# Performance work log

Hardware: AMD Instinct MI355X
Metric: run time of the kernel (lower is better)

The kernel has to match this reference:

```python
import jax, jax.numpy as jnp
import numpy as np

B, D, H, W, C_IN, F = 32, 8, 8, 8, 512, 96
KS = (3, 3, 3)


def setup_inputs() -> dict:
    key = jax.random.key(0)
    ks = jax.random.split(key, 12)
    sc_w = 0.05  # keras 'random_uniform' is small; scale keeps activations sane
    inp = {
        "inputs": jax.random.normal(ks[0], (B, C_IN), jnp.float32),
        "h_t": jax.random.normal(ks[1], (B, D, H, W, F), jnp.float32),
        "s_t": jax.random.normal(ks[2], (B, D, H, W, F), jnp.float32),
        "Wf": jax.random.uniform(ks[3], (D, H, W, C_IN, F), jnp.float32, -sc_w, sc_w),
        "Wi": jax.random.uniform(ks[4], (D, H, W, C_IN, F), jnp.float32, -sc_w, sc_w),
        "Ws": jax.random.uniform(ks[5], (D, H, W, C_IN, F), jnp.float32, -sc_w, sc_w),
        "Uf": jax.random.normal(ks[6], KS + (F, F), jnp.float32) * 0.05,
        "Ui": jax.random.normal(ks[7], KS + (F, F), jnp.float32) * 0.05,
        "Us": jax.random.normal(ks[8], KS + (F, F), jnp.float32) * 0.05,
        "bf": jnp.zeros((F,), jnp.float32),
        "bi": jnp.zeros((F,), jnp.float32),
        "bs": jnp.zeros((F,), jnp.float32),
    }
    return inp


def _conv3d_same(h, U):
    # channels_last 3D conv, stride 1, SAME padding (matches K.conv3d)
    return jax.lax.conv_general_dilated(
        h, U, window_strides=(1, 1, 1), padding="SAME",
        dimension_numbers=("NDHWC", "DHWIO", "NDHWC"))


def _hard_sigmoid(x):
    # keras hard_sigmoid: clip(0.2*x + 0.5, 0, 1)
    return jnp.clip(0.2 * x + 0.5, 0.0, 1.0)


def reference(inputs, h_t, s_t, Wf, Uf, Wi, Ui, Ws, Us, bf, bi, bs):
    # K.dot(inputs, W): contract input channel c against W's second-to-last axis
    def gate(Wg, Ug, bg):
        return jnp.einsum("bc,dhwcf->bdhwf", inputs, Wg) + _conv3d_same(h_t, Ug) + bg

    f = _hard_sigmoid(gate(Wf, Uf, bf))
    i = _hard_sigmoid(gate(Wi, Ui, bi))
    s = f * s_t + i * jnp.tanh(gate(Ws, Us, bs))
    h = jnp.tanh(s)
    return (h, s)
```

## Files before the change

### kernel.cpp

```cpp
#include <hip/hip_runtime.h>

typedef __attribute__((ext_vector_type(8))) short short8;
typedef __attribute__((ext_vector_type(4))) float f32x4;

constexpr int B_ = 32, C_ = 512, F_ = 96, P_ = 512;
constexpr int NTH = 768;
constexpr int GRID = 256;
constexpr size_t OUT_HALF = (size_t)B_ * P_ * F_;

constexpr size_t WS_U  = 0;
constexpr size_t WS_U_SZ = 27ull * 3 * 96 * 52 * 4;
constexpr size_t WS_H  = WS_U + WS_U_SZ;
constexpr size_t WS_H_SZ = 32ull * 512 * 96 * 2;
constexpr size_t WS_X  = WS_H + WS_H_SZ;
constexpr size_t WS_X_SZ = 32ull * 512 * 2;
constexpr size_t WS_END = WS_X + WS_X_SZ;

constexpr int SH_OFF = 0;
constexpr int SH_BUF = 64 * 208;
constexpr int SU_OFF = SH_OFF + 2 * SH_BUF;
constexpr int SU_BUF = 3 * 96 * 208;
constexpr int LDS_TOTAL = SU_OFF + 2 * SU_BUF;
constexpr int SX_OFF = 0;
constexpr int SW_OFF = 33280;
constexpr int SW_BUF = 6 * 96 * 80;
constexpr int PRE_OFF = 0;

__device__ __forceinline__ unsigned short f2bf(float v) {
    unsigned int u = __float_as_uint(v);
    unsigned int r = (u + 0x7FFFu + ((u >> 16) & 1u)) >> 16;
    return (unsigned short)r;
}
__device__ __forceinline__ unsigned pack2bf(float a, float b) {
    return (unsigned)f2bf(a) | ((unsigned)f2bf(b) << 16);
}
__device__ __forceinline__ float bf2f(unsigned short v) {
    return __uint_as_float(((unsigned int)v) << 16);
}

__global__ __launch_bounds__(256) void prep_u(const float* __restrict__ Uf,
                                              const float* __restrict__ Ui,
                                              const float* __restrict__ Us,
                                              unsigned char* __restrict__ wsb) {
    __shared__ float s32[96 * 97];
    const int t = blockIdx.x / 3, g = blockIdx.x % 3;
    const float* U = (g == 0 ? Uf : (g == 1 ? Ui : Us)) + (size_t)t * 9216;
    const int tid = threadIdx.x;
    #pragma unroll
    for (int j = 0; j < 36; ++j) {
        int idx = j * 256 + tid;
        int ci = idx / 96, f = idx % 96;
        s32[ci * 97 + f] = U[idx];
    }
    __syncthreads();
    unsigned* dst = (unsigned*)(wsb + WS_U) + (size_t)(t * 3 + g) * 4992;
    #pragma unroll
    for (int j = 0; j < 20; ++j) {
        int o = j * 256 + tid;
        if (o < 4992) {
            int f = o / 52, qq = o % 52;
            unsigned pk = 0u;
            if (qq < 48) pk = pack2bf(s32[(2 * qq) * 97 + f], s32[(2 * qq + 1) * 97 + f]);
            dst[o] = pk;
        }
    }
}

__global__ __launch_bounds__(256) void prep_hx(const float* __restrict__ h_t,
                                               const float* __restrict__ x,
                                               unsigned char* __restrict__ wsb) {
    unsigned* wh = (unsigned*)(wsb + WS_H);
    unsigned* wx = (unsigned*)(wsb + WS_X);
    const int tid = threadIdx.x;
    #pragma unroll
    for (int j = 0; j < 4; ++j) {
        size_t u = (size_t)blockIdx.x * 1024 + j * 256 + tid;
        if (u < 786432) {
            float2 v = *(const float2*)(h_t + 2 * u);
            wh[u] = pack2bf(v.x, v.y);
        } else if (u < 794624) {
            size_t v_ = u - 786432;
            float2 v = *(const float2*)(x + 2 * v_);
            wx[v_] = pack2bf(v.x, v.y);
        }
    }
}

__global__ __launch_bounds__(NTH, 3) void lstm3d_main(
    const float* __restrict__ Wf, const float* __restrict__ Wi, const float* __restrict__ Ws,
    const float* __restrict__ s_t,
    const float* __restrict__ bfp, const float* __restrict__ bip, const float* __restrict__ bsp,
    const unsigned char* __restrict__ wsb, float* __restrict__ out)
{
    extern __shared__ char sm[];
    const int tid  = threadIdx.x;
    const int lane = tid & 63;
    const int wv   = tid >> 6;
    const int kp   = (wv >= 6) ? 1 : 0;
    const int w6   = kp ? wv - 6 : wv;
    const int g    = w6 >> 1;
    const int m    = w6 & 1;
    const int l15  = lane & 15, l4 = lane >> 4;

    const int bid = blockIdx.x;
    const int w0  = (bid & 3) * 2;
    const int dh  = bid >> 2;
    const int dd  = dh >> 3, hh = dh & 7;
    const int p0  = dd * 64 + hh * 8 + w0;

    const unsigned char* wh8 = wsb + WS_H;
    const unsigned char* wu8 = wsb + WS_U;
    const unsigned char* wx8 = wsb + WS_X;

    f32x4 acc[2][6];
    #pragma unroll
    for (int a = 0; a < 2; ++a)
        #pragma unroll
        for (int b = 0; b < 6; ++b) acc[a][b] = (f32x4){0.f, 0.f, 0.f, 0.f};

    const int hrow = tid / 12;
    const int hgq  = tid % 12;
    const int hhalf = hrow >> 5, hb = hrow & 31;

    auto tap_info = [&](int kt, int& np0, int& np1, int& a0, int& a1) {
        int kd = kt / 9, kh = (kt / 3) % 3, kw = kt % 3;
        int nd = dd + kd - 1, nh = hh + kh - 1;
        int nwA = w0 + kw - 1, nwB = nwA + 1;
        int ok = ((unsigned)nd < 8u) && ((unsigned)nh < 8u);
        a0 = ok && ((unsigned)nwA < 8u);
        a1 = ok && ((unsigned)nwB < 8u);
        np0 = nd * 64 + nh * 8 + nwA;
        np1 = nd * 64 + nh * 8 + nwB;
    };

    int kt = 0, np0 = 0, np1 = 0, a0 = 0, a1 = 0;
    for (; kt < 27; ++kt) { tap_info(kt, np0, np1, a0, a1); if (a0 | a1) break; }

    {
        uint4 hv = {0u, 0u, 0u, 0u};
        int np = hhalf ? np1 : np0;
        int av = hhalf ? a1 : a0;
        if (av) hv = *(const uint4*)(wh8 + (size_t)hb * 98304 + np * 192 + hgq * 16);
        *(uint4*)(sm + SH_OFF + hrow * 208 + hgq * 16) = hv;
        #pragma unroll
        for (int j = 0; j < 5; ++j) {
            int gi = j * 768 + tid;
            if (gi < 3744) {
                uint4 uv = *(const uint4*)(wu8 + (size_t)kt * 59904 + gi * 16);
                *(uint4*)(sm + SU_OFF + gi * 16) = uv;
            }
        }
    }
    __syncthreads();

    int buf = 0, actIdx = 0;
    while (kt < 27) {
        int ktn = kt + 1, np0n = 0, np1n = 0, a0n = 0, a1n = 0;
        for (; ktn < 27; ++ktn) { tap_info(ktn, np0n, np1n, a0n, a1n); if (a0n | a1n) break; }
        const bool havenext = (ktn < 27);

        uint4 hv = {0u, 0u, 0u, 0u};
        uint4 uv0, uv1, uv2, uv3, uv4;
        if (havenext) {
            int np = hhalf ? np1n : np0n;
            int av = hhalf ? a1n : a0n;
            if (av) hv = *(const uint4*)(wh8 + (size_t)hb * 98304 + np * 192 + hgq * 16);
            const unsigned char* ub = wu8 + (size_t)ktn * 59904;
            uv0 = *(const uint4*)(ub + (0 * 768 + tid) * 16);
            uv1 = *(const uint4*)(ub + (1 * 768 + tid) * 16);
            uv2 = *(const uint4*)(ub + (2 * 768 + tid) * 16);
            uv3 = *(const uint4*)(ub + (3 * 768 + tid) * 16);
            if (4 * 768 + tid < 3744) uv4 = *(const uint4*)(ub + (4 * 768 + tid) * 16);
        }

        {
            const char* shb = sm + SH_OFF + buf * SH_BUF;
            const char* sub = sm + SU_OFF + buf * SU_BUF + g * 19968;
            #pragma unroll
            for (int ks = 0; ks < 3; ++ks) {
                if (((actIdx * 3 + ks) & 1) != kp) continue;
                short8 afr0 = *(const short8*)(shb + (m * 32 + l15) * 208      + ks * 64 + l4 * 16);
                short8 afr1 = *(const short8*)(shb + (m * 32 + 16 + l15) * 208 + ks * 64 + l4 * 16);
                #pragma unroll
                for (int n = 0; n < 6; ++n) {
                    short8 bfr = *(const short8*)(sub + (n * 16 + l15) * 208 + ks * 64 + l4 * 16);
                    acc[0][n] = __builtin_amdgcn_mfma_f32_16x16x32_bf16(afr0, bfr, acc[0][n], 0, 0, 0);
                    acc[1][n] = __builtin_amdgcn_mfma_f32_16x16x32_bf16(afr1, bfr, acc[1][n], 0, 0, 0);
                }
            }
        }

        if (havenext) {
            *(uint4*)(sm + SH_OFF + (buf ^ 1) * SH_BUF + hrow * 208 + hgq * 16) = hv;
            char* sb = sm + SU_OFF + (buf ^ 1) * SU_BUF;
            *(uint4*)(sb + (0 * 768 + tid) * 16) = uv0;
            *(uint4*)(sb + (1 * 768 + tid) * 16) = uv1;
            *(uint4*)(sb + (2 * 768 + tid) * 16) = uv2;
            *(uint4*)(sb + (3 * 768 + tid) * 16) = uv3;
            if (4 * 768 + tid < 3744) *(uint4*)(sb + (4 * 768 + tid) * 16) = uv4;
        }
        __syncthreads();
        buf ^= 1; ++actIdx;
        kt = ktn; np0 = np0n; np1 = np1n; a0 = a0n; a1 = a1n;
    }

    #pragma unroll
    for (int j = 0; j < 3; ++j) {
        int gi = j * 768 + tid;
        if (gi < 2048) {
            int row = gi >> 6, gg = gi & 63;
            uint4 v = *(const uint4*)(wx8 + row * 1024 + gg * 16);
            *(uint4*)(sm + SX_OFF + row * 1040 + gg * 16) = v;
        }
    }

    const int rA = tid, rB = 768 + tid;
    const int qA = rA / 96, fA = rA % 96;
    const int qB = rB / 96, fB = rB % 96;

    float2 wvv[12];
    #pragma unroll
    for (int j = 0; j < 12; ++j) {
        const int s  = j >> 1;
        const int sg = s >> 1;
        const int sp = s & 1;
        const int q  = (j & 1) ? qB : qA;
        const int f  = (j & 1) ? fB : fA;
        const float* W = (sg == 0) ? Wf : ((sg == 1) ? Wi : Ws);
        size_t base = ((size_t)(p0 + sp) * 512 + 2 * q) * 96 + f;
        wvv[j].x = W[base];
        wvv[j].y = W[base + 96];
    }
    #pragma unroll
    for (int j = 0; j < 12; ++j) {
        const int s = j >> 1;
        const int q = (j & 1) ? qB : qA;
        const int f = (j & 1) ? fB : fA;
        *(unsigned*)(sm + SW_OFF + s * 7680 + f * 80 + q * 4) = pack2bf(wvv[j].x, wvv[j].y);
    }
    __syncthreads();

    buf = 0;
    for (int ks = 0; ks < 16; ++ks) {
        const bool havenext = (ks + 1) < 16;
        if (havenext) {
            const int c0n = (ks + 1) * 32;
            #pragma unroll
            for (int j = 0; j < 12; ++j) {
                const int s  = j >> 1;
                const int sg = s >> 1;
                const int sp = s & 1;
                const int q  = (j & 1) ? qB : qA;
                const int f  = (j & 1) ? fB : fA;
                const float* W = (sg == 0) ? Wf : ((sg == 1) ? Wi : Ws);
                size_t base = ((size_t)(p0 + sp) * 512 + c0n + 2 * q) * 96 + f;
                wvv[j].x = W[base];
                wvv[j].y = W[base + 96];
            }
        }

        if ((ks & 1) == kp) {
            const char* sxb = sm + SX_OFF;
            const char* swb = sm + SW_OFF + buf * SW_BUF + (g * 2 + m) * 7680;
            short8 afr0 = *(const short8*)(sxb + (l15) * 1040      + ks * 64 + l4 * 16);
            short8 afr1 = *(const short8*)(sxb + (16 + l15) * 1040 + ks * 64 + l4 * 16);
            #pragma unroll
            for (int n = 0; n < 6; ++n) {
                short8 bfr = *(const short8*)(swb + (n * 16 + l15) * 80 + l4 * 16);
                acc[0][n] = __builtin_amdgcn_mfma_f32_16x16x32_bf16(afr0, bfr, acc[0][n], 0, 0, 0);
                acc[1][n] = __builtin_amdgcn_mfma_f32_16x16x32_bf16(afr1, bfr, acc[1][n], 0, 0, 0);
            }
        }

        if (havenext) {
            #pragma unroll
            for (int j = 0; j < 12; ++j) {
                const int s = j >> 1;
                const int q = (j & 1) ? qB : qA;
                const int f = (j & 1) ? fB : fA;
                *(unsigned*)(sm + SW_OFF + (buf ^ 1) * SW_BUF + s * 7680 + f * 80 + q * 4) =
                    pack2bf(wvv[j].x, wvv[j].y);
            }
        }
        __syncthreads();
        buf ^= 1;
    }

    float* pre = (float*)(sm + PRE_OFF);
    const int preBase = (m * 3 + g) * 32 * 96;
    if (kp == 1) {
        #pragma unroll
        for (int ti = 0; ti < 2; ++ti)
            #pragma unroll
            for (int n = 0; n < 6; ++n)
                #pragma unroll
                for (int r = 0; r < 4; ++r)
                    pre[preBase + (ti * 16 + l4 * 4 + r) * 96 + n * 16 + l15] = acc[ti][n][r];
    }
    __syncthreads();
    if (kp == 0) {
        #pragma unroll
        for (int ti = 0; ti < 2; ++ti)
            #pragma unroll
            for (int n = 0; n < 6; ++n)
                #pragma unroll
                for (int r = 0; r < 4; ++r)
                    pre[preBase + (ti * 16 + l4 * 4 + r) * 96 + n * 16 + l15] += acc[ti][n][r];
    }
    __syncthreads();

    #pragma unroll
    for (int j = 0; j < 8; ++j) {
        int u  = j * 768 + tid;
        int mm = u / 3072;
        int rr = (u / 96) % 32;
        int ff = u % 96;
        float gfv = pre[((mm * 3 + 0) * 32 + rr) * 96 + ff] + bfp[ff];
        float giv = pre[((mm * 3 + 1) * 32 + rr) * 96 + ff] + bip[ff];
        float gsv = pre[((mm * 3 + 2) * 32 + rr) * 96 + ff] + bsp[ff];
        int pg = p0 + mm;
        size_t idx = ((size_t)rr * 512 + pg) * 96 + ff;
        float fg = fminf(fmaxf(0.2f * gfv + 0.5f, 0.f), 1.f);
        float ig = fminf(fmaxf(0.2f * giv + 0.5f, 0.f), 1.f);
        float sv = fg * s_t[idx] + ig * tanhf(gsv);
        out[idx] = tanhf(sv);
        out[OUT_HALF + idx] = sv;
    }
}

constexpr int FNTH = 384;
constexpr int FBPG = 8;
__global__ __launch_bounds__(FNTH, 3) void lstm3d_fused(
    const float* __restrict__ x, const float* __restrict__ h_t, const float* __restrict__ s_t,
    const float* __restrict__ Wf, const float* __restrict__ Wi, const float* __restrict__ Ws,
    const float* __restrict__ Uf, const float* __restrict__ Ui, const float* __restrict__ Us,
    const float* __restrict__ bf, const float* __restrict__ bi, const float* __restrict__ bs,
    float* __restrict__ out)
{
    __shared__ __align__(16) unsigned char lds_raw[B_*C_*2 + B_*F_*4];
    unsigned short* s_in = (unsigned short*)lds_raw;
    float*          s_h  = (float*)(lds_raw + B_*C_*2);
    const int p = blockIdx.x, d = p >> 6, hh = (p >> 3) & 7, ww = p & 7;
    const int tid = threadIdx.x, f = tid % F_, bg = tid / F_, b0 = bg * FBPG;
    {
        const float4* x4 = (const float4*)x;
        ushort4* s4 = (ushort4*)s_in;
        for (int i = tid; i < B_ * C_ / 4; i += FNTH) {
            float4 v = x4[i];
            ushort4 u; u.x = f2bf(v.x); u.y = f2bf(v.y); u.z = f2bf(v.z); u.w = f2bf(v.w);
            s4[i] = u;
        }
    }
    __syncthreads();
    const size_t wbase = (size_t)p * C_ * F_;
    const float* Wfp = Wf + wbase; const float* Wip = Wi + wbase; const float* Wsp = Ws + wbase;
    float af[FBPG], ai[FBPG], as_[FBPG];
    #pragma unroll
    for (int j = 0; j < FBPG; ++j) { af[j] = 0.f; ai[j] = 0.f; as_[j] = 0.f; }
    for (int c = 0; c < C_; c += 4) {
        float xs[FBPG][4];
        #pragma unroll
        for (int j = 0; j < FBPG; ++j) {
            ushort4 uv = *(const ushort4*)&s_in[(b0 + j) * C_ + c];
            xs[j][0] = bf2f(uv.x); xs[j][1] = bf2f(uv.y); xs[j][2] = bf2f(uv.z); xs[j][3] = bf2f(uv.w);
        }
        #pragma unroll
        for (int cc = 0; cc < 4; ++cc) {
            const float wfv = Wfp[(c + cc) * F_ + f], wiv = Wip[(c + cc) * F_ + f], wsv = Wsp[(c + cc) * F_ + f];
            #pragma unroll
            for (int j = 0; j < FBPG; ++j) {
                af[j] = fmaf(xs[j][cc], wfv, af[j]); ai[j] = fmaf(xs[j][cc], wiv, ai[j]); as_[j] = fmaf(xs[j][cc], wsv, as_[j]);
            }
        }
    }
    float cf[FBPG], cig[FBPG], cs[FBPG];
    #pragma unroll
    for (int j = 0; j < FBPG; ++j) { cf[j] = 0.f; cig[j] = 0.f; cs[j] = 0.f; }
    for (int kd = 0; kd < 3; ++kd) {
        const int nd = d + kd - 1; if ((unsigned)nd >= 8u) continue;
        for (int kh = 0; kh < 3; ++kh) {
            const int nh = hh + kh - 1; if ((unsigned)nh >= 8u) continue;
            for (int kw = 0; kw < 3; ++kw) {
                const int nw = ww + kw - 1; if ((unsigned)nw >= 8u) continue;
                const int np = (nd << 6) + (nh << 3) + nw, k = (kd * 3 + kh) * 3 + kw;
                __syncthreads();
                {
                    const float4* h4 = (const float4*)h_t; float4* s4 = (float4*)s_h;
                    for (int i = tid; i < B_ * F_ / 4; i += FNTH) {
                        const int b2 = i / (F_ / 4), r = i % (F_ / 4);
                        s4[i] = h4[(size_t)(b2 * P_ + np) * (F_ / 4) + r];
                    }
                }
                __syncthreads();
                const float* Ufk = Uf + (size_t)k * F_ * F_; const float* Uik = Ui + (size_t)k * F_ * F_; const float* Usk = Us + (size_t)k * F_ * F_;
                for (int ci = 0; ci < F_; ci += 4) {
                    float hs[FBPG][4];
                    #pragma unroll
                    for (int j = 0; j < FBPG; ++j) {
                        float4 t = *(const float4*)&s_h[(b0 + j) * F_ + ci];
                        hs[j][0] = t.x; hs[j][1] = t.y; hs[j][2] = t.z; hs[j][3] = t.w;
                    }
                    #pragma unroll
                    for (int cc = 0; cc < 4; ++cc) {
                        const float ufv = Ufk[(ci + cc) * F_ + f], uiv = Uik[(ci + cc) * F_ + f], usv = Usk[(ci + cc) * F_ + f];
                        #pragma unroll
                        for (int j = 0; j < FBPG; ++j) {
                            cf[j] = fmaf(hs[j][cc], ufv, cf[j]); cig[j] = fmaf(hs[j][cc], uiv, cig[j]); cs[j] = fmaf(hs[j][cc], usv, cs[j]);
                        }
                    }
                }
            }
        }
    }
    const float bfv = bf[f], biv = bi[f], bsv = bs[f];
    #pragma unroll
    for (int j = 0; j < FBPG; ++j) {
        const size_t idx = (size_t)((b0 + j) * P_ + p) * F_ + f;
        const float gf = af[j] + cf[j] + bfv, gi = ai[j] + cig[j] + biv, gs = as_[j] + cs[j] + bsv;
        const float fg = fminf(fmaxf(0.2f * gf + 0.5f, 0.f), 1.f);
        const float ig = fminf(fmaxf(0.2f * gi + 0.5f, 0.f), 1.f);
        const float sv = fg * s_t[idx] + ig * tanhf(gs);
        out[idx] = tanhf(sv);
        out[OUT_HALF + idx] = sv;
    }
}

extern "C" void kernel_launch(void* const* d_in, const int* in_sizes, int n_in,
                              void* d_out, int out_size, void* d_ws, size_t ws_size,
                              hipStream_t stream) {
    const float* x   = (const float*)d_in[0];
    const float* h_t = (const float*)d_in[1];
    const float* s_t = (const float*)d_in[2];
    const float* Wf  = (const float*)d_in[3];
    const float* Wi  = (const float*)d_in[4];
    const float* Ws  = (const float*)d_in[5];
    const float* Uf  = (const float*)d_in[6];
    const float* Ui  = (const float*)d_in[7];
    const float* Us  = (const float*)d_in[8];
    const float* bf  = (const float*)d_in[9];
    const float* bi  = (const float*)d_in[10];
    const float* bs  = (const float*)d_in[11];
    float* out = (float*)d_out;

    if (ws_size >= WS_END) {
        (void)hipFuncSetAttribute(reinterpret_cast<const void*>(lstm3d_main),
                                  hipFuncAttributeMaxDynamicSharedMemorySize, LDS_TOTAL);
        unsigned char* wsb = (unsigned char*)d_ws;
        hipLaunchKernelGGL(prep_u, dim3(81), dim3(256), 0, stream, Uf, Ui, Us, wsb);
        hipLaunchKernelGGL(prep_hx, dim3(776), dim3(256), 0, stream, h_t, x, wsb);
        hipLaunchKernelGGL(lstm3d_main, dim3(GRID), dim3(NTH), LDS_TOTAL, stream,
                           Wf, Wi, Ws, s_t, bf, bi, bs, wsb, out);
    } else {
        hipLaunchKernelGGL(lstm3d_fused, dim3(P_), dim3(FNTH), 0, stream,
                           x, h_t, s_t, Wf, Wi, Ws, Uf, Ui, Us, bf, bi, bs, out);
    }
}
```

Measured before the change: 110.2 us.

## Rework main kernel to one spatial position per block with 32x32 MFMA tiles

```diff
diff --git a/kernel.cpp b/kernel.cpp
--- a/kernel.cpp
+++ b/kernel.cpp
@@ -2,10 +2,11 @@
 
 typedef __attribute__((ext_vector_type(8))) short short8;
 typedef __attribute__((ext_vector_type(4))) float f32x4;
+typedef __attribute__((ext_vector_type(16))) float f32x16;
 
 constexpr int B_ = 32, C_ = 512, F_ = 96, P_ = 512;
-constexpr int NTH = 768;
-constexpr int GRID = 256;
+constexpr int NTH = 576;
+constexpr int GRID = 512;
 constexpr size_t OUT_HALF = (size_t)B_ * P_ * F_;
 
 constexpr size_t WS_U  = 0;
@@ -16,15 +17,12 @@
 constexpr size_t WS_X_SZ = 32ull * 512 * 2;
 constexpr size_t WS_END = WS_X + WS_X_SZ;
 
-constexpr int SH_OFF = 0;
-constexpr int SH_BUF = 64 * 208;
-constexpr int SU_OFF = SH_OFF + 2 * SH_BUF;
-constexpr int SU_BUF = 3 * 96 * 208;
-constexpr int LDS_TOTAL = SU_OFF + 2 * SU_BUF;
-constexpr int SX_OFF = 0;
-constexpr int SW_OFF = 33280;
-constexpr int SW_BUF = 6 * 96 * 80;
-constexpr int PRE_OFF = 0;
+constexpr int X_OFF    = 0;
+constexpr int X_STRIDE = 1040;
+constexpr int H_OFF    = 33280;
+constexpr int WT_OFF   = H_OFF + 32 * 208;
+constexpr int WT_BUF   = 3 * 96 * 48;
+constexpr int LDS_TOTAL = WT_OFF + 2 * WT_BUF;
 
 __device__ __forceinline__ unsigned short f2bf(float v) {
     unsigned int u = __float_as_uint(v);
@@ -86,7 +84,7 @@
     }
 }
 
-__global__ __launch_bounds__(NTH, 3) void lstm3d_main(
+__global__ __launch_bounds__(NTH, 5) void lstm3d_main(
     const float* __restrict__ Wf, const float* __restrict__ Wi, const float* __restrict__ Ws,
     const float* __restrict__ s_t,
     const float* __restrict__ bfp, const float* __restrict__ bip, const float* __restrict__ bsp,
@@ -96,235 +94,133 @@
     const int tid  = threadIdx.x;
     const int lane = tid & 63;
     const int wv   = tid >> 6;
-    const int kp   = (wv >= 6) ? 1 : 0;
-    const int w6   = kp ? wv - 6 : wv;
-    const int g    = w6 >> 1;
-    const int m    = w6 & 1;
-    const int l15  = lane & 15, l4 = lane >> 4;
-
-    const int bid = blockIdx.x;
-    const int w0  = (bid & 3) * 2;
-    const int dh  = bid >> 2;
-    const int dd  = dh >> 3, hh = dh & 7;
-    const int p0  = dd * 64 + hh * 8 + w0;
+    const int g    = wv / 3;
+    const int n    = wv % 3;
+    const int l31  = lane & 31, l5 = lane >> 5;
+
+    const int p  = blockIdx.x;
+    const int dd = p >> 6, hh = (p >> 3) & 7, ww = p & 7;
 
     const unsigned char* wh8 = wsb + WS_H;
     const unsigned char* wu8 = wsb + WS_U;
     const unsigned char* wx8 = wsb + WS_X;
 
-    f32x4 acc[2][6];
-    #pragma unroll
-    for (int a = 0; a < 2; ++a)
-        #pragma unroll
-        for (int b = 0; b < 6; ++b) acc[a][b] = (f32x4){0.f, 0.f, 0.f, 0.f};
-
-    const int hrow = tid / 12;
-    const int hgq  = tid % 12;
-    const int hhalf = hrow >> 5, hb = hrow & 31;
-
-    auto tap_info = [&](int kt, int& np0, int& np1, int& a0, int& a1) {
-        int kd = kt / 9, kh = (kt / 3) % 3, kw = kt % 3;
-        int nd = dd + kd - 1, nh = hh + kh - 1;
-        int nwA = w0 + kw - 1, nwB = nwA + 1;
-        int ok = ((unsigned)nd < 8u) && ((unsigned)nh < 8u);
-        a0 = ok && ((unsigned)nwA < 8u);
-        a1 = ok && ((unsigned)nwB < 8u);
-        np0 = nd * 64 + nh * 8 + nwA;
-        np1 = nd * 64 + nh * 8 + nwB;
+    f32x16 acc;
+    #pragma unroll
+    for (int r = 0; r < 16; ++r) acc[r] = 0.f;
+
+    #pragma unroll
+    for (int i0 = 0; i0 < 4; ++i0) {
+        int i = i0 * NTH + tid;
+        if (i < 2048) {
+            int row = i >> 6, gq = i & 63;
+            *(uint4*)(sm + X_OFF + row * X_STRIDE + gq * 16) =
+                *(const uint4*)(wx8 + row * 1024 + gq * 16);
+        }
+    }
+    __syncthreads();
+
+    auto do_conv = [&]() {
+        const unsigned char* ubrow_base = wu8 + (size_t)(g * 96 + n * 32 + l31) * 208;
+        for (int kt = 0; kt < 27; ++kt) {
+            const int kd = kt / 9, kh = (kt / 3) % 3, kw = kt % 3;
+            const int nd = dd + kd - 1, nh = hh + kh - 1, nw = ww + kw - 1;
+            if ((unsigned)nd >= 8u || (unsigned)nh >= 8u || (unsigned)nw >= 8u) continue;
+            const int np = nd * 64 + nh * 8 + nw;
+
+            uint4 hv;
+            const int hb = tid / 12, hq = tid % 12;
+            if (tid < 384)
+                hv = *(const uint4*)(wh8 + (size_t)hb * 98304 + np * 192 + hq * 16);
+            uint4 bb[6];
+            const unsigned char* ub = ubrow_base + (size_t)kt * (3 * 96 * 208);
+            #pragma unroll
+            for (int ks = 0; ks < 6; ++ks)
+                bb[ks] = *(const uint4*)(ub + ks * 32 + l5 * 16);
+
+            __syncthreads();
+            if (tid < 384)
+                *(uint4*)(sm + H_OFF + hb * 208 + hq * 16) = hv;
+            __syncthreads();
+
+            #pragma unroll
+            for (int ks = 0; ks < 6; ++ks) {
+                short8 a = *(const short8*)(sm + H_OFF + l31 * 208 + ks * 32 + l5 * 16);
+                short8 b = __builtin_bit_cast(short8, bb[ks]);
+                acc = __builtin_amdgcn_mfma_f32_32x32x16_bf16(a, b, acc, 0, 0, 0);
+            }
+        }
     };
 
-    int kt = 0, np0 = 0, np1 = 0, a0 = 0, a1 = 0;
-    for (; kt < 27; ++kt) { tap_info(kt, np0, np1, a0, a1); if (a0 | a1) break; }
-
-    {
-        uint4 hv = {0u, 0u, 0u, 0u};
-        int np = hhalf ? np1 : np0;
-        int av = hhalf ? a1 : a0;
-        if (av) hv = *(const uint4*)(wh8 + (size_t)hb * 98304 + np * 192 + hgq * 16);
-        *(uint4*)(sm + SH_OFF + hrow * 208 + hgq * 16) = hv;
-        #pragma unroll
-        for (int j = 0; j < 5; ++j) {
-            int gi = j * 768 + tid;
-            if (gi < 3744) {
-                uint4 uv = *(const uint4*)(wu8 + (size_t)kt * 59904 + gi * 16);
-                *(uint4*)(sm + SU_OFF + gi * 16) = uv;
-            }
-        }
-    }
-    __syncthreads();
-
-    int buf = 0, actIdx = 0;
-    while (kt < 27) {
-        int ktn = kt + 1, np0n = 0, np1n = 0, a0n = 0, a1n = 0;
-        for (; ktn < 27; ++ktn) { tap_info(ktn, np0n, np1n, a0n, a1n); if (a0n | a1n) break; }
-        const bool havenext = (ktn < 27);
-
-        uint4 hv = {0u, 0u, 0u, 0u};
-        uint4 uv0, uv1, uv2, uv3, uv4;
-        if (havenext) {
-            int np = hhalf ? np1n : np0n;
-            int av = hhalf ? a1n : a0n;
-            if (av) hv = *(const uint4*)(wh8 + (size_t)hb * 98304 + np * 192 + hgq * 16);
-            const unsigned char* ub = wu8 + (size_t)ktn * 59904;
-            uv0 = *(const uint4*)(ub + (0 * 768 + tid) * 16);
-            uv1 = *(const uint4*)(ub + (1 * 768 + tid) * 16);
-            uv2 = *(const uint4*)(ub + (2 * 768 + tid) * 16);
-            uv3 = *(const uint4*)(ub + (3 * 768 + tid) * 16);
-            if (4 * 768 + tid < 3744) uv4 = *(const uint4*)(ub + (4 * 768 + tid) * 16);
-        }
-
-        {
-            const char* shb = sm + SH_OFF + buf * SH_BUF;
-            const char* sub = sm + SU_OFF + buf * SU_BUF + g * 19968;
-            #pragma unroll
-            for (int ks = 0; ks < 3; ++ks) {
-                if (((actIdx * 3 + ks) & 1) != kp) continue;
-                short8 afr0 = *(const short8*)(shb + (m * 32 + l15) * 208      + ks * 64 + l4 * 16);
-                short8 afr1 = *(const short8*)(shb + (m * 32 + 16 + l15) * 208 + ks * 64 + l4 * 16);
-                #pragma unroll
-                for (int n = 0; n < 6; ++n) {
-                    short8 bfr = *(const short8*)(sub + (n * 16 + l15) * 208 + ks * 64 + l4 * 16);
-                    acc[0][n] = __builtin_amdgcn_mfma_f32_16x16x32_bf16(afr0, bfr, acc[0][n], 0, 0, 0);
-                    acc[1][n] = __builtin_amdgcn_mfma_f32_16x16x32_bf16(afr1, bfr, acc[1][n], 0, 0, 0);
-                }
-            }
-        }
-
-        if (havenext) {
-            *(uint4*)(sm + SH_OFF + (buf ^ 1) * SH_BUF + hrow * 208 + hgq * 16) = hv;
-            char* sb = sm + SU_OFF + (buf ^ 1) * SU_BUF;
-            *(uint4*)(sb + (0 * 768 + tid) * 16) = uv0;
-            *(uint4*)(sb + (1 * 768 + tid) * 16) = uv1;
-            *(uint4*)(sb + (2 * 768 + tid) * 16) = uv2;
-            *(uint4*)(sb + (3 * 768 + tid) * 16) = uv3;
-            if (4 * 768 + tid < 3744) *(uint4*)(sb + (4 * 768 + tid) * 16) = uv4;
-        }
-        __syncthreads();
-        buf ^= 1; ++actIdx;
-        kt = ktn; np0 = np0n; np1 = np1n; a0 = a0n; a1 = a1n;
-    }
-
-    #pragma unroll
-    for (int j = 0; j < 3; ++j) {
-        int gi = j * 768 + tid;
-        if (gi < 2048) {
-            int row = gi >> 6, gg = gi & 63;
-            uint4 v = *(const uint4*)(wx8 + row * 1024 + gg * 16);
-            *(uint4*)(sm + SX_OFF + row * 1040 + gg * 16) = v;
-        }
-    }
-
-    const int rA = tid, rB = 768 + tid;
-    const int qA = rA / 96, fA = rA % 96;
-    const int qB = rB / 96, fB = rB % 96;
-
-    float2 wvv[12];
-    #pragma unroll
-    for (int j = 0; j < 12; ++j) {
-        const int s  = j >> 1;
-        const int sg = s >> 1;
-        const int sp = s & 1;
-        const int q  = (j & 1) ? qB : qA;
-        const int f  = (j & 1) ? fB : fA;
-        const float* W = (sg == 0) ? Wf : ((sg == 1) ? Wi : Ws);
-        size_t base = ((size_t)(p0 + sp) * 512 + 2 * q) * 96 + f;
-        wvv[j].x = W[base];
-        wvv[j].y = W[base + 96];
-    }
-    #pragma unroll
-    for (int j = 0; j < 12; ++j) {
-        const int s = j >> 1;
-        const int q = (j & 1) ? qB : qA;
-        const int f = (j & 1) ? fB : fA;
-        *(unsigned*)(sm + SW_OFF + s * 7680 + f * 80 + q * 4) = pack2bf(wvv[j].x, wvv[j].y);
-    }
-    __syncthreads();
-
-    buf = 0;
-    for (int ks = 0; ks < 16; ++ks) {
-        const bool havenext = (ks + 1) < 16;
-        if (havenext) {
-            const int c0n = (ks + 1) * 32;
-            #pragma unroll
-            for (int j = 0; j < 12; ++j) {
-                const int s  = j >> 1;
-                const int sg = s >> 1;
-                const int sp = s & 1;
-                const int q  = (j & 1) ? qB : qA;
-                const int f  = (j & 1) ? fB : fA;
-                const float* W = (sg == 0) ? Wf : ((sg == 1) ? Wi : Ws);
-                size_t base = ((size_t)(p0 + sp) * 512 + c0n + 2 * q) * 96 + f;
-                wvv[j].x = W[base];
-                wvv[j].y = W[base + 96];
-            }
-        }
-
-        if ((ks & 1) == kp) {
-            const char* sxb = sm + SX_OFF;
-            const char* swb = sm + SW_OFF + buf * SW_BUF + (g * 2 + m) * 7680;
-            short8 afr0 = *(const short8*)(sxb + (l15) * 1040      + ks * 64 + l4 * 16);
-            short8 afr1 = *(const short8*)(sxb + (16 + l15) * 1040 + ks * 64 + l4 * 16);
-            #pragma unroll
-            for (int n = 0; n < 6; ++n) {
-                short8 bfr = *(const short8*)(swb + (n * 16 + l15) * 80 + l4 * 16);
-                acc[0][n] = __builtin_amdgcn_mfma_f32_16x16x32_bf16(afr0, bfr, acc[0][n], 0, 0, 0);
-                acc[1][n] = __builtin_amdgcn_mfma_f32_16x16x32_bf16(afr1, bfr, acc[1][n], 0, 0, 0);
-            }
-        }
-
-        if (havenext) {
-            #pragma unroll
-            for (int j = 0; j < 12; ++j) {
-                const int s = j >> 1;
-                const int q = (j & 1) ? qB : qA;
-                const int f = (j & 1) ? fB : fA;
-                *(unsigned*)(sm + SW_OFF + (buf ^ 1) * SW_BUF + s * 7680 + f * 80 + q * 4) =
-                    pack2bf(wvv[j].x, wvv[j].y);
-            }
-        }
-        __syncthreads();
-        buf ^= 1;
-    }
-
-    float* pre = (float*)(sm + PRE_OFF);
-    const int preBase = (m * 3 + g) * 32 * 96;
-    if (kp == 1) {
-        #pragma unroll
-        for (int ti = 0; ti < 2; ++ti)
-            #pragma unroll
-            for (int n = 0; n < 6; ++n)
-                #pragma unroll
-                for (int r = 0; r < 4; ++r)
-                    pre[preBase + (ti * 16 + l4 * 4 + r) * 96 + n * 16 + l15] = acc[ti][n][r];
-    }
-    __syncthreads();
-    if (kp == 0) {
-        #pragma unroll
-        for (int ti = 0; ti < 2; ++ti)
-            #pragma unroll
-            for (int n = 0; n < 6; ++n)
-                #pragma unroll
-                for (int r = 0; r < 4; ++r)
-                    pre[preBase + (ti * 16 + l4 * 4 + r) * 96 + n * 16 + l15] += acc[ti][n][r];
-    }
-    __syncthreads();
-
-    #pragma unroll
-    for (int j = 0; j < 8; ++j) {
-        int u  = j * 768 + tid;
-        int mm = u / 3072;
-        int rr = (u / 96) % 32;
-        int ff = u % 96;
-        float gfv = pre[((mm * 3 + 0) * 32 + rr) * 96 + ff] + bfp[ff];
-        float giv = pre[((mm * 3 + 1) * 32 + rr) * 96 + ff] + bip[ff];
-        float gsv = pre[((mm * 3 + 2) * 32 + rr) * 96 + ff] + bsp[ff];
-        int pg = p0 + mm;
-        size_t idx = ((size_t)rr * 512 + pg) * 96 + ff;
-        float fg = fminf(fmaxf(0.2f * gfv + 0.5f, 0.f), 1.f);
-        float ig = fminf(fmaxf(0.2f * giv + 0.5f, 0.f), 1.f);
-        float sv = fg * s_t[idx] + ig * tanhf(gsv);
-        out[idx] = tanhf(sv);
-        out[OUT_HALF + idx] = sv;
+    auto do_proj = [&]() {
+        const int tq = tid / 96, f_ = tid % 96;
+
+        float wlA[8], wlB[8];
+        auto issue = [&](int k, float (&wl)[8]) {
+            const int c0 = k * 16;
+            #pragma unroll
+            for (int q = 0; q < 4; ++q) {
+                const int rest = q * 6 + tq;
+                const int cp = rest & 7, gg = rest >> 3;
+                const float* W = (gg == 0) ? Wf : ((gg == 1) ? Wi : Ws);
+                const size_t base = ((size_t)p * 512 + c0 + 2 * cp) * 96 + f_;
+                wl[2 * q]     = W[base];
+                wl[2 * q + 1] = W[base + 96];
+            }
+        };
+        auto phase = [&](int k, float (&wl)[8]) {
+            unsigned wp[4];
+            #pragma unroll
+            for (int q = 0; q < 4; ++q) wp[q] = pack2bf(wl[2 * q], wl[2 * q + 1]);
+            if (k + 2 < 32) issue(k + 2, wl);
+            char* wb = sm + WT_OFF + (k & 1) * WT_BUF;
+            #pragma unroll
+            for (int q = 0; q < 4; ++q) {
+                const int rest = q * 6 + tq;
+                const int cp = rest & 7, gg = rest >> 3;
+                *(unsigned*)(wb + (gg * 96 + f_) * 48 + cp * 4) = wp[q];
+            }
+            __syncthreads();
+            short8 a = *(const short8*)(sm + X_OFF + l31 * X_STRIDE + k * 32 + l5 * 16);
+            short8 b = *(const short8*)(wb + (g * 96 + n * 32 + l31) * 48 + l5 * 16);
+            acc = __builtin_amdgcn_mfma_f32_32x32x16_bf16(a, b, acc, 0, 0, 0);
+        };
+
+        issue(0, wlA);
+        issue(1, wlB);
+        for (int k2 = 0; k2 < 16; ++k2) {
+            phase(2 * k2,     wlA);
+            phase(2 * k2 + 1, wlB);
+        }
+    };
+
+    if ((blockIdx.x >> 3) & 1) { do_proj(); do_conv(); }
+    else                       { do_conv(); do_proj(); }
+
+    __syncthreads();
+    float* pre = (float*)sm;
+    #pragma unroll
+    for (int r = 0; r < 16; ++r) {
+        const int b = (r & 3) + 8 * (r >> 2) + 4 * l5;
+        pre[(g * 32 + b) * 96 + n * 32 + l31] = acc[r];
+    }
+    __syncthreads();
+
+    #pragma unroll
+    for (int j = 0; j < 6; ++j) {
+        const int i = j * NTH + tid;
+        if (i < 3072) {
+            const int b = i / 96, f = i % 96;
+            const float gfv = pre[(0 * 32 + b) * 96 + f] + bfp[f];
+            const float giv = pre[(1 * 32 + b) * 96 + f] + bip[f];
+            const float gsv = pre[(2 * 32 + b) * 96 + f] + bsp[f];
+            const size_t idx = ((size_t)b * 512 + p) * 96 + f;
+            const float fg = fminf(fmaxf(0.2f * gfv + 0.5f, 0.f), 1.f);
+            const float ig = fminf(fmaxf(0.2f * giv + 0.5f, 0.f), 1.f);
+            const float sv = fg * s_t[idx] + ig * tanhf(gsv);
+            out[idx] = tanhf(sv);
+            out[OUT_HALF + idx] = sv;
+        }
     }
 }
 
```

Measured after the change: 195.3 us. +77.3%, slower.
